# Kernel tuning notes

Hardware: AMD Instinct MI355X
Metric: run time of the kernel (lower is better)

## Reference

```python
import jax, jax.numpy as jnp
import numpy as np

N, E, F, H = 50000, 400000, 128, 512


def setup_inputs() -> dict:
    key = jax.random.key(0)
    k1, k2, k3 = jax.random.split(key, 3)
    x = jax.random.normal(k1, (N, F), dtype=jnp.float32)
    edge_index = jax.random.randint(k2, (2, E), 0, N, dtype=jnp.int64)
    W = jax.random.normal(k3, (H, F), dtype=jnp.float32) * 0.05  # GCNConv linear weight [out, in]
    b = jnp.zeros((H,), dtype=jnp.float32)
    alpha = jnp.full((H,), 0.25, dtype=jnp.float32)  # PReLU default init per channel
    return {"x": x, "edge_index": edge_index, "W": W, "b": b, "alpha": alpha}


def reference(x, edge_index, W, b, alpha):
    n = x.shape[0]
    # GCNConv: linear transform first (no bias inside the matmul)
    h = x @ W.T  # [N, H]
    # add self-loops (GCNConv default add_self_loops=True)
    loops = jnp.arange(n, dtype=edge_index.dtype)
    row = jnp.concatenate([edge_index[0], loops])  # source
    col = jnp.concatenate([edge_index[1], loops])  # target
    # symmetric degree normalization: deg from edge weights (all ones) summed at targets
    deg = jax.ops.segment_sum(jnp.ones_like(col, dtype=h.dtype), col, num_segments=n)
    dinv = jnp.where(deg > 0, jax.lax.rsqrt(jnp.maximum(deg, 1.0)) * (deg > 0), 0.0)
    dinv = jnp.where(deg > 0, 1.0 / jnp.sqrt(jnp.maximum(deg, 1e-12)), 0.0)
    norm = dinv[row] * dinv[col]  # [E+N]
    # gather source features, scale, scatter-add to targets
    msgs = h[row] * norm[:, None]  # [E+N, H] -- the memory-bound gather
    out = jax.ops.segment_sum(msgs, col, num_segments=n) + b  # [N, H]
    # PReLU with per-channel alpha
    return jnp.where(out > 0, out, alpha * out)
```

## Files before the change

kernel.cpp:

```cpp
#include <hip/hip_runtime.h>


#define F_IN 128
#define H_OUT 512

typedef __bf16 bf16x8 __attribute__((ext_vector_type(8)));
typedef float  f32x4  __attribute__((ext_vector_type(4)));

__global__ __launch_bounds__(256) void prep_kernel(const float* __restrict__ W,
                                                   __bf16* __restrict__ Wb, int nw8,
                                                   const float* __restrict__ x,
                                                   __bf16* __restrict__ xs, int nx8,
                                                   const int* __restrict__ col,
                                                   unsigned* __restrict__ deg,
                                                   unsigned* __restrict__ pos, int E,
                                                   int NWB, int NXB) {
    const int b = blockIdx.x, t = threadIdx.x;
    if (b < NWB) {
        int i = b * 256 + t;
        if (i >= nw8) return;
        float4 a0 = ((const float4*)W)[i * 2];
        float4 a1 = ((const float4*)W)[i * 2 + 1];
        bf16x8 v;
        v[0] = (__bf16)a0.x; v[1] = (__bf16)a0.y; v[2] = (__bf16)a0.z; v[3] = (__bf16)a0.w;
        v[4] = (__bf16)a1.x; v[5] = (__bf16)a1.y; v[6] = (__bf16)a1.z; v[7] = (__bf16)a1.w;
        ((bf16x8*)Wb)[i] = v;
    } else if (b < NWB + NXB) {
        int i = (b - NWB) * 256 + t;
        if (i >= nx8) return;
        float4 a0 = ((const float4*)x)[i * 2];
        float4 a1 = ((const float4*)x)[i * 2 + 1];
        bf16x8 v;
        v[0] = (__bf16)a0.x; v[1] = (__bf16)a0.y; v[2] = (__bf16)a0.z; v[3] = (__bf16)a0.w;
        v[4] = (__bf16)a1.x; v[5] = (__bf16)a1.y; v[6] = (__bf16)a1.z; v[7] = (__bf16)a1.w;
        ((bf16x8*)xs)[i] = v;
    } else {
        int e = (b - NWB - NXB) * 256 + t;
        if (e < E) pos[e] = atomicAdd(&deg[col[e]], 1u);
    }
}

__global__ __launch_bounds__(256) void assign_kernel(const unsigned* __restrict__ deg,
                                                     unsigned* __restrict__ total,
                                                     int* __restrict__ rowptr,
                                                     float* __restrict__ dinv, int n) {
    const int i = blockIdx.x * 256 + threadIdx.x;
    const int lane = threadIdx.x & 63;
    unsigned d = (i < n) ? deg[i] : 0u;
    unsigned da = (d + 7u) & ~7u;
    unsigned x = da;
    #pragma unroll
    for (int o = 1; o < 64; o <<= 1) {
        unsigned y = __shfl_up(x, (unsigned)o, 64);
        if (lane >= o) x += y;
    }
    unsigned tot = __shfl(x, 63, 64);
    unsigned wb = 0;
    if (lane == 63) wb = atomicAdd(total, tot);
    wb = __shfl(wb, 63, 64);
    if (i < n) {
        rowptr[i] = (int)(wb + x - da);
        dinv[i]   = rsqrtf((float)(d + 1u));
    }
}

__global__ __launch_bounds__(256) void fill_csr_kernel(const int* __restrict__ row,
                                                       const int* __restrict__ col,
                                                       const unsigned* __restrict__ pos,
                                                       const int* __restrict__ rowptr,
                                                       int* __restrict__ adj, int E) {
    int e = blockIdx.x * 256 + threadIdx.x;
    if (e >= E) return;
    adj[rowptr[col[e]] + (int)pos[e]] = row[e];
}

__global__ __launch_bounds__(256) void gather_agg_kernel(const int* __restrict__ rowptr,
                                                         const unsigned* __restrict__ deg,
                                                         const int* __restrict__ adj,
                                                         const __bf16* __restrict__ xs,
                                                         const float* __restrict__ dinv,
                                                         __bf16* __restrict__ ag, int N) {
    const int t = threadIdx.x;
    const int node = blockIdx.x * 16 + (t >> 4);
    if (node >= N) return;
    const int li = t & 15;

    const bf16x8* xs8 = (const bf16x8*)xs;
    const float dvn = dinv[node];
    bf16x8 sv = xs8[(size_t)node * 16 + li];
    float acc[8];
    #pragma unroll
    for (int q = 0; q < 8; ++q) acc[q] = dvn * (float)sv[q];

    const int s = rowptr[node];
    const int e = s + (int)deg[node];
    for (int j = s; j < e; j += 8) {
        int4 ra = *(const int4*)(adj + j);
        int4 rb = *(const int4*)(adj + j + 4);
        int rr[8];
        rr[0] = ra.x; rr[1] = ra.y; rr[2] = ra.z; rr[3] = ra.w;
        rr[4] = rb.x; rr[5] = rb.y; rr[6] = rb.z; rr[7] = rb.w;
        float wgt[8]; bf16x8 v[8];
        #pragma unroll
        for (int u = 0; u < 8; ++u) {
            const bool ok = (j + u) < e;
            const int r = ok ? rr[u] : node;
            wgt[u] = ok ? dinv[r] : 0.0f;
            v[u]   = xs8[(size_t)r * 16 + li];
        }
        #pragma unroll
        for (int u = 0; u < 8; ++u) {
            #pragma unroll
            for (int q = 0; q < 8; ++q) acc[q] += wgt[u] * (float)v[u][q];
        }
    }

    bf16x8 o;
    #pragma unroll
    for (int q = 0; q < 8; ++q) o[q] = (__bf16)(acc[q] * dvn);
    ((bf16x8*)ag)[(size_t)node * 16 + li] = o;
}

__global__ __launch_bounds__(256) void gemm_mfma_kernel(const __bf16* __restrict__ ag,
                                                        const __bf16* __restrict__ Wb,
                                                        const float* __restrict__ bias,
                                                        const float* __restrict__ alpha,
                                                        float* __restrict__ out, int N) {
    __shared__ __bf16 As[128][136];
    __shared__ __bf16 Bs[128][136];

    const int rb = blockIdx.x * 128;
    const int cb = blockIdx.y * 128;
    const int t  = threadIdx.x;

    #pragma unroll
    for (int i = 0; i < 8; ++i) {
        int c  = i * 256 + t;
        int r  = c >> 4;
        int k8 = (c & 15) * 8;
        bf16x8 v;
        #pragma unroll
        for (int j = 0; j < 8; ++j) v[j] = (__bf16)0.0f;
        if (rb + r < N) v = *(const bf16x8*)(ag + (size_t)(rb + r) * F_IN + k8);
        *(bf16x8*)&As[r][k8] = v;
    }
    #pragma unroll
    for (int i = 0; i < 8; ++i) {
        int c  = i * 256 + t;
        int r  = c >> 4;
        int k8 = (c & 15) * 8;
        bf16x8 v = *(const bf16x8*)(Wb + (size_t)(cb + r) * F_IN + k8);
        *(bf16x8*)&Bs[r][k8] = v;
    }
    __syncthreads();

    const int w    = t >> 6;
    const int lane = t & 63;
    const int lrow = lane & 15;
    const int lk   = (lane >> 4) * 8;

    f32x4 acc[2][8] = {};
    #pragma unroll
    for (int ks = 0; ks < 4; ++ks) {
        const int k0 = ks * 32 + lk;
        bf16x8 a0 = *(const bf16x8*)&As[w * 32 + lrow][k0];
        bf16x8 a1 = *(const bf16x8*)&As[w * 32 + 16 + lrow][k0];
        #pragma unroll
        for (int tn = 0; tn < 8; ++tn) {
            bf16x8 bfr = *(const bf16x8*)&Bs[tn * 16 + lrow][k0];
            acc[0][tn] = __builtin_amdgcn_mfma_f32_16x16x32_bf16(a0, bfr, acc[0][tn], 0, 0, 0);
            acc[1][tn] = __builtin_amdgcn_mfma_f32_16x16x32_bf16(a1, bfr, acc[1][tn], 0, 0, 0);
        }
    }

    float bb[8], aa[8];
    #pragma unroll
    for (int tn = 0; tn < 8; ++tn) {
        int n = cb + tn * 16 + lrow;
        bb[tn] = bias[n];
        aa[tn] = alpha[n];
    }
    const int rloc = (lane >> 4) * 4;
    #pragma unroll
    for (int tm = 0; tm < 2; ++tm) {
        #pragma unroll
        for (int r = 0; r < 4; ++r) {
            int m = rb + w * 32 + tm * 16 + rloc + r;
            if (m >= N) continue;
            #pragma unroll
            for (int tn = 0; tn < 8; ++tn) {
                int n = cb + tn * 16 + lrow;
                float v = acc[tm][tn][r] + bb[tn];
                v = v > 0.f ? v : aa[tn] * v;
                out[(size_t)m * H_OUT + n] = v;
            }
        }
    }
}

extern "C" void kernel_launch(void* const* d_in, const int* in_sizes, int n_in,
                              void* d_out, int out_size, void* d_ws, size_t ws_size,
                              hipStream_t stream) {
    const float* x     = (const float*)d_in[0];
    const int*   ei    = (const int*)d_in[1];
    const float* W     = (const float*)d_in[2];
    const float* b     = (const float*)d_in[3];
    const float* alpha = (const float*)d_in[4];
    float*       out   = (float*)d_out;

    const int N = in_sizes[0] / F_IN;
    const int E = in_sizes[1] / 2;
    const int* row = ei;
    const int* col = ei + E;

    char* wsb = (char*)d_ws;
    size_t off = 0;
    __bf16* xs = (__bf16*)(wsb + off);  off += (size_t)N * F_IN * 2;     off = (off + 63) & ~(size_t)63;
    __bf16* ag = (__bf16*)(wsb + off);  off += (size_t)N * F_IN * 2;     off = (off + 63) & ~(size_t)63;
    __bf16* Wb = (__bf16*)(wsb + off);  off += (size_t)H_OUT * F_IN * 2; off = (off + 63) & ~(size_t)63;
    unsigned* deg    = (unsigned*)(wsb + off);  off += (size_t)(N + 1) * 4;
    float*    dinv   = (float*)(wsb + off);     off += (size_t)N * 4;
    int*      rowptr = (int*)(wsb + off);       off += (size_t)N * 4;
    off = (off + 63) & ~(size_t)63;
    unsigned* pos = (unsigned*)(wsb + off);     off += (size_t)E * 4;
    off = (off + 63) & ~(size_t)63;
    int* adj = (int*)(wsb + off);
    unsigned* total = deg + N;

    const int nw8 = H_OUT * F_IN / 8;
    const int nx8 = N * F_IN / 8;
    const int NWB = (nw8 + 255) / 256;
    const int NXB = (nx8 + 255) / 256;
    const int NEB = (E + 255) / 256;

    hipMemsetAsync(deg, 0, (size_t)(N + 1) * 4, stream);
    prep_kernel<<<NWB + NXB + NEB, 256, 0, stream>>>(W, Wb, nw8, x, xs, nx8,
                                                     col, deg, pos, E, NWB, NXB);
    assign_kernel<<<(N + 255) / 256, 256, 0, stream>>>(deg, total, rowptr, dinv, N);
    fill_csr_kernel<<<(E + 255) / 256, 256, 0, stream>>>(row, col, pos, rowptr, adj, E);
    gather_agg_kernel<<<(N + 15) / 16, 256, 0, stream>>>(rowptr, deg, adj, xs, dinv, ag, N);
    dim3 ggrid((N + 127) / 128, H_OUT / 128);
    gemm_mfma_kernel<<<ggrid, 256, 0, stream>>>(ag, Wb, b, alpha, out, N);
}
```

Measured before the change: 210.7 us.

## Fuse neighbor aggregation into the MFMA GEMM, keeping aggregated rows in LDS

The separate gather-aggregate kernel and GEMM kernel are merged. Each 128-row block aggregates its nodes' neighbor features straight into shared memory, then loops over all four 128-column weight tiles, producing every output column for those rows. This removes the bf16 intermediate write and read to global memory plus one launch, and each aggregated tile is read once instead of four times. In exchange the grid shrinks to about 391 blocks doing serialized gather work, which lowers parallelism and latency hiding for the irregular gather, and W tiles are reloaded per block.

```diff
diff --git a/kernel.cpp b/kernel.cpp
--- a/kernel.cpp
+++ b/kernel.cpp
@@ -74,83 +74,61 @@
     adj[rowptr[col[e]] + (int)pos[e]] = row[e];
 }
 
-__global__ __launch_bounds__(256) void gather_agg_kernel(const int* __restrict__ rowptr,
-                                                         const unsigned* __restrict__ deg,
-                                                         const int* __restrict__ adj,
-                                                         const __bf16* __restrict__ xs,
-                                                         const float* __restrict__ dinv,
-                                                         __bf16* __restrict__ ag, int N) {
-    const int t = threadIdx.x;
-    const int node = blockIdx.x * 16 + (t >> 4);
-    if (node >= N) return;
-    const int li = t & 15;
-
-    const bf16x8* xs8 = (const bf16x8*)xs;
-    const float dvn = dinv[node];
-    bf16x8 sv = xs8[(size_t)node * 16 + li];
-    float acc[8];
-    #pragma unroll
-    for (int q = 0; q < 8; ++q) acc[q] = dvn * (float)sv[q];
-
-    const int s = rowptr[node];
-    const int e = s + (int)deg[node];
-    for (int j = s; j < e; j += 8) {
-        int4 ra = *(const int4*)(adj + j);
-        int4 rb = *(const int4*)(adj + j + 4);
-        int rr[8];
-        rr[0] = ra.x; rr[1] = ra.y; rr[2] = ra.z; rr[3] = ra.w;
-        rr[4] = rb.x; rr[5] = rb.y; rr[6] = rb.z; rr[7] = rb.w;
-        float wgt[8]; bf16x8 v[8];
-        #pragma unroll
-        for (int u = 0; u < 8; ++u) {
-            const bool ok = (j + u) < e;
-            const int r = ok ? rr[u] : node;
-            wgt[u] = ok ? dinv[r] : 0.0f;
-            v[u]   = xs8[(size_t)r * 16 + li];
-        }
-        #pragma unroll
-        for (int u = 0; u < 8; ++u) {
-            #pragma unroll
-            for (int q = 0; q < 8; ++q) acc[q] += wgt[u] * (float)v[u][q];
-        }
-    }
-
-    bf16x8 o;
-    #pragma unroll
-    for (int q = 0; q < 8; ++q) o[q] = (__bf16)(acc[q] * dvn);
-    ((bf16x8*)ag)[(size_t)node * 16 + li] = o;
-}
-
-__global__ __launch_bounds__(256) void gemm_mfma_kernel(const __bf16* __restrict__ ag,
-                                                        const __bf16* __restrict__ Wb,
-                                                        const float* __restrict__ bias,
-                                                        const float* __restrict__ alpha,
-                                                        float* __restrict__ out, int N) {
+__global__ __launch_bounds__(256) void fused_agg_gemm_kernel(
+        const int* __restrict__ rowptr, const unsigned* __restrict__ deg,
+        const int* __restrict__ adj, const __bf16* __restrict__ xs,
+        const float* __restrict__ dinv, const __bf16* __restrict__ Wb,
+        const float* __restrict__ bias, const float* __restrict__ alpha,
+        float* __restrict__ out, int N) {
     __shared__ __bf16 As[128][136];
     __shared__ __bf16 Bs[128][136];
 
     const int rb = blockIdx.x * 128;
-    const int cb = blockIdx.y * 128;
     const int t  = threadIdx.x;
-
-    #pragma unroll
-    for (int i = 0; i < 8; ++i) {
-        int c  = i * 256 + t;
-        int r  = c >> 4;
-        int k8 = (c & 15) * 8;
-        bf16x8 v;
-        #pragma unroll
-        for (int j = 0; j < 8; ++j) v[j] = (__bf16)0.0f;
-        if (rb + r < N) v = *(const bf16x8*)(ag + (size_t)(rb + r) * F_IN + k8);
-        *(bf16x8*)&As[r][k8] = v;
-    }
-    #pragma unroll
-    for (int i = 0; i < 8; ++i) {
-        int c  = i * 256 + t;
-        int r  = c >> 4;
-        int k8 = (c & 15) * 8;
-        bf16x8 v = *(const bf16x8*)(Wb + (size_t)(cb + r) * F_IN + k8);
-        *(bf16x8*)&Bs[r][k8] = v;
+    const int li   = t & 15;
+    const int slot = t >> 4;
+
+    const bf16x8* xs8 = (const bf16x8*)xs;
+
+    for (int nl = slot; nl < 128; nl += 16) {
+        const int node = rb + nl;
+        bf16x8 o;
+        if (node < N) {
+            const float dvn = dinv[node];
+            bf16x8 sv = xs8[(size_t)node * 16 + li];
+            float acc[8];
+            #pragma unroll
+            for (int q = 0; q < 8; ++q) acc[q] = dvn * (float)sv[q];
+
+            const int s = rowptr[node];
+            const int e = s + (int)deg[node];
+            for (int j = s; j < e; j += 8) {
+                int4 ra = *(const int4*)(adj + j);
+                int4 rb4 = *(const int4*)(adj + j + 4);
+                int rr[8];
+                rr[0] = ra.x;  rr[1] = ra.y;  rr[2] = ra.z;  rr[3] = ra.w;
+                rr[4] = rb4.x; rr[5] = rb4.y; rr[6] = rb4.z; rr[7] = rb4.w;
+                float wgt[8]; bf16x8 v[8];
+                #pragma unroll
+                for (int u = 0; u < 8; ++u) {
+                    const bool ok = (j + u) < e;
+                    const int r = ok ? rr[u] : node;
+                    wgt[u] = ok ? dinv[r] : 0.0f;
+                    v[u]   = xs8[(size_t)r * 16 + li];
+                }
+                #pragma unroll
+                for (int u = 0; u < 8; ++u) {
+                    #pragma unroll
+                    for (int q = 0; q < 8; ++q) acc[q] += wgt[u] * (float)v[u][q];
+                }
+            }
+            #pragma unroll
+            for (int q = 0; q < 8; ++q) o[q] = (__bf16)(acc[q] * dvn);
+        } else {
+            #pragma unroll
+            for (int q = 0; q < 8; ++q) o[q] = (__bf16)0.0f;
+        }
+        *(bf16x8*)&As[nl][li * 8] = o;
     }
     __syncthreads();
 
@@ -158,41 +136,61 @@
     const int lane = t & 63;
     const int lrow = lane & 15;
     const int lk   = (lane >> 4) * 8;
-
-    f32x4 acc[2][8] = {};
+    const int rloc = (lane >> 4) * 4;
+
+    bf16x8 af0[4], af1[4];
     #pragma unroll
     for (int ks = 0; ks < 4; ++ks) {
         const int k0 = ks * 32 + lk;
-        bf16x8 a0 = *(const bf16x8*)&As[w * 32 + lrow][k0];
-        bf16x8 a1 = *(const bf16x8*)&As[w * 32 + 16 + lrow][k0];
+        af0[ks] = *(const bf16x8*)&As[w * 32 + lrow][k0];
+        af1[ks] = *(const bf16x8*)&As[w * 32 + 16 + lrow][k0];
+    }
+
+    for (int ct = 0; ct < 4; ++ct) {
+        const int cb = ct * 128;
+        __syncthreads();
+        #pragma unroll
+        for (int i = 0; i < 8; ++i) {
+            int c  = i * 256 + t;
+            int r  = c >> 4;
+            int k8 = (c & 15) * 8;
+            bf16x8 v = *(const bf16x8*)(Wb + (size_t)(cb + r) * F_IN + k8);
+            *(bf16x8*)&Bs[r][k8] = v;
+        }
+        __syncthreads();
+
+        f32x4 acc[2][8] = {};
+        #pragma unroll
+        for (int ks = 0; ks < 4; ++ks) {
+            const int k0 = ks * 32 + lk;
+            #pragma unroll
+            for (int tn = 0; tn < 8; ++tn) {
+                bf16x8 bfr = *(const bf16x8*)&Bs[tn * 16 + lrow][k0];
+                acc[0][tn] = __builtin_amdgcn_mfma_f32_16x16x32_bf16(af0[ks], bfr, acc[0][tn], 0, 0, 0);
+                acc[1][tn] = __builtin_amdgcn_mfma_f32_16x16x32_bf16(af1[ks], bfr, acc[1][tn], 0, 0, 0);
+            }
+        }
+
+        float bb[8], aa[8];
         #pragma unroll
         for (int tn = 0; tn < 8; ++tn) {
-            bf16x8 bfr = *(const bf16x8*)&Bs[tn * 16 + lrow][k0];
-            acc[0][tn] = __builtin_amdgcn_mfma_f32_16x16x32_bf16(a0, bfr, acc[0][tn], 0, 0, 0);
-            acc[1][tn] = __builtin_amdgcn_mfma_f32_16x16x32_bf16(a1, bfr, acc[1][tn], 0, 0, 0);
-        }
-    }
-
-    float bb[8], aa[8];
-    #pragma unroll
-    for (int tn = 0; tn < 8; ++tn) {
-        int n = cb + tn * 16 + lrow;
-        bb[tn] = bias[n];
-        aa[tn] = alpha[n];
-    }
-    const int rloc = (lane >> 4) * 4;
-    #pragma unroll
-    for (int tm = 0; tm < 2; ++tm) {
-        #pragma unroll
-        for (int r = 0; r < 4; ++r) {
-            int m = rb + w * 32 + tm * 16 + rloc + r;
-            if (m >= N) continue;
-            #pragma unroll
-            for (int tn = 0; tn < 8; ++tn) {
-                int n = cb + tn * 16 + lrow;
-                float v = acc[tm][tn][r] + bb[tn];
-                v = v > 0.f ? v : aa[tn] * v;
-                out[(size_t)m * H_OUT + n] = v;
+            int n = cb + tn * 16 + lrow;
+            bb[tn] = bias[n];
+            aa[tn] = alpha[n];
+        }
+        #pragma unroll
+        for (int tm = 0; tm < 2; ++tm) {
+            #pragma unroll
+            for (int r = 0; r < 4; ++r) {
+                int m = rb + w * 32 + tm * 16 + rloc + r;
+                if (m >= N) continue;
+                #pragma unroll
+                for (int tn = 0; tn < 8; ++tn) {
+                    int n = cb + tn * 16 + lrow;
+                    float v = acc[tm][tn][r] + bb[tn];
+                    v = v > 0.f ? v : aa[tn] * v;
+                    out[(size_t)m * H_OUT + n] = v;
+                }
             }
         }
     }
@@ -216,7 +214,6 @@
     char* wsb = (char*)d_ws;
     size_t off = 0;
     __bf16* xs = (__bf16*)(wsb + off);  off += (size_t)N * F_IN * 2;     off = (off + 63) & ~(size_t)63;
-    __bf16* ag = (__bf16*)(wsb + off);  off += (size_t)N * F_IN * 2;     off = (off + 63) & ~(size_t)63;
     __bf16* Wb = (__bf16*)(wsb + off);  off += (size_t)H_OUT * F_IN * 2; off = (off + 63) & ~(size_t)63;
     unsigned* deg    = (unsigned*)(wsb + off);  off += (size_t)(N + 1) * 4;
     float*    dinv   = (float*)(wsb + off);     off += (size_t)N * 4;
@@ -238,7 +235,6 @@
                                                      col, deg, pos, E, NWB, NXB);
     assign_kernel<<<(N + 255) / 256, 256, 0, stream>>>(deg, total, rowptr, dinv, N);
     fill_csr_kernel<<<(E + 255) / 256, 256, 0, stream>>>(row, col, pos, rowptr, adj, E);
-    gather_agg_kernel<<<(N + 15) / 16, 256, 0, stream>>>(rowptr, deg, adj, xs, dinv, ag, N);
-    dim3 ggrid((N + 127) / 128, H_OUT / 128);
-    gemm_mfma_kernel<<<ggrid, 256, 0, stream>>>(ag, Wb, b, alpha, out, N);
-}
+    fused_agg_gemm_kernel<<<(N + 127) / 128, 256, 0, stream>>>(
+        rowptr, deg, adj, xs, dinv, Wb, b, alpha, out, N);
+}
```

Measured after the change: 213.3 us. Within noise of the previous version (+1.2%).

## Loop over all output column tiles per GEMM block, reusing A fragments

Applied to the files above, without the earlier changes.

The GEMM grid drops its column dimension. Each block now loads its 128-row A tile once, keeps the A fragments in registers, and loops over the four 128-column W tiles, reloading Bs in shared memory between passes. This removes the fourfold re-read of the aggregated activations and uses nontemporal stores for the large fp32 output. In exchange there are 4x fewer blocks (about 391), less parallelism to hide latency, and extra barriers around the serial W reloads.

```diff
diff --git a/kernel.cpp b/kernel.cpp
--- a/kernel.cpp
+++ b/kernel.cpp
@@ -95,11 +95,11 @@
     const int s = rowptr[node];
     const int e = s + (int)deg[node];
     for (int j = s; j < e; j += 8) {
-        int4 ra = *(const int4*)(adj + j);
-        int4 rb = *(const int4*)(adj + j + 4);
+        int4 ra  = *(const int4*)(adj + j);
+        int4 rb4 = *(const int4*)(adj + j + 4);
         int rr[8];
-        rr[0] = ra.x; rr[1] = ra.y; rr[2] = ra.z; rr[3] = ra.w;
-        rr[4] = rb.x; rr[5] = rb.y; rr[6] = rb.z; rr[7] = rb.w;
+        rr[0] = ra.x;  rr[1] = ra.y;  rr[2] = ra.z;  rr[3] = ra.w;
+        rr[4] = rb4.x; rr[5] = rb4.y; rr[6] = rb4.z; rr[7] = rb4.w;
         float wgt[8]; bf16x8 v[8];
         #pragma unroll
         for (int u = 0; u < 8; ++u) {
@@ -130,7 +130,6 @@
     __shared__ __bf16 Bs[128][136];
 
     const int rb = blockIdx.x * 128;
-    const int cb = blockIdx.y * 128;
     const int t  = threadIdx.x;
 
     #pragma unroll
@@ -149,8 +148,7 @@
         int c  = i * 256 + t;
         int r  = c >> 4;
         int k8 = (c & 15) * 8;
-        bf16x8 v = *(const bf16x8*)(Wb + (size_t)(cb + r) * F_IN + k8);
-        *(bf16x8*)&Bs[r][k8] = v;
+        *(bf16x8*)&Bs[r][k8] = *(const bf16x8*)(Wb + (size_t)r * F_IN + k8);
     }
     __syncthreads();
 
@@ -158,42 +156,66 @@
     const int lane = t & 63;
     const int lrow = lane & 15;
     const int lk   = (lane >> 4) * 8;
-
-    f32x4 acc[2][8] = {};
+    const int rloc = (lane >> 4) * 4;
+
+    bf16x8 af0[4], af1[4];
     #pragma unroll
     for (int ks = 0; ks < 4; ++ks) {
         const int k0 = ks * 32 + lk;
-        bf16x8 a0 = *(const bf16x8*)&As[w * 32 + lrow][k0];
-        bf16x8 a1 = *(const bf16x8*)&As[w * 32 + 16 + lrow][k0];
+        af0[ks] = *(const bf16x8*)&As[w * 32 + lrow][k0];
+        af1[ks] = *(const bf16x8*)&As[w * 32 + 16 + lrow][k0];
+    }
+
+    #pragma unroll
+    for (int ct = 0; ct < 4; ++ct) {
+        const int cb = ct * 128;
+
+        f32x4 acc[2][8] = {};
+        #pragma unroll
+        for (int ks = 0; ks < 4; ++ks) {
+            const int k0 = ks * 32 + lk;
+            #pragma unroll
+            for (int tn = 0; tn < 8; ++tn) {
+                bf16x8 bfr = *(const bf16x8*)&Bs[tn * 16 + lrow][k0];
+                acc[0][tn] = __builtin_amdgcn_mfma_f32_16x16x32_bf16(af0[ks], bfr, acc[0][tn], 0, 0, 0);
+                acc[1][tn] = __builtin_amdgcn_mfma_f32_16x16x32_bf16(af1[ks], bfr, acc[1][tn], 0, 0, 0);
+            }
+        }
+
+        float bb[8], aa[8];
         #pragma unroll
         for (int tn = 0; tn < 8; ++tn) {
-            bf16x8 bfr = *(const bf16x8*)&Bs[tn * 16 + lrow][k0];
-            acc[0][tn] = __builtin_amdgcn_mfma_f32_16x16x32_bf16(a0, bfr, acc[0][tn], 0, 0, 0);
-            acc[1][tn] = __builtin_amdgcn_mfma_f32_16x16x32_bf16(a1, bfr, acc[1][tn], 0, 0, 0);
-        }
-    }
-
-    float bb[8], aa[8];
-    #pragma unroll
-    for (int tn = 0; tn < 8; ++tn) {
-        int n = cb + tn * 16 + lrow;
-        bb[tn] = bias[n];
-        aa[tn] = alpha[n];
-    }
-    const int rloc = (lane >> 4) * 4;
-    #pragma unroll
-    for (int tm = 0; tm < 2; ++tm) {
-        #pragma unroll
-        for (int r = 0; r < 4; ++r) {
-            int m = rb + w * 32 + tm * 16 + rloc + r;
-            if (m >= N) continue;
-            #pragma unroll
-            for (int tn = 0; tn < 8; ++tn) {
-                int n = cb + tn * 16 + lrow;
-                float v = acc[tm][tn][r] + bb[tn];
-                v = v > 0.f ? v : aa[tn] * v;
-                out[(size_t)m * H_OUT + n] = v;
+            int n = cb + tn * 16 + lrow;
+            bb[tn] = bias[n];
+            aa[tn] = alpha[n];
+        }
+        #pragma unroll
+        for (int tm = 0; tm < 2; ++tm) {
+            #pragma unroll
+            for (int r = 0; r < 4; ++r) {
+                int m = rb + w * 32 + tm * 16 + rloc + r;
+                if (m >= N) continue;
+                #pragma unroll
+                for (int tn = 0; tn < 8; ++tn) {
+                    int n = cb + tn * 16 + lrow;
+                    float v = acc[tm][tn][r] + bb[tn];
+                    v = v > 0.f ? v : aa[tn] * v;
+                    __builtin_nontemporal_store(v, &out[(size_t)m * H_OUT + n]);
+                }
             }
+        }
+
+        if (ct < 3) {
+            __syncthreads();
+            #pragma unroll
+            for (int i = 0; i < 8; ++i) {
+                int c  = i * 256 + t;
+                int r  = c >> 4;
+                int k8 = (c & 15) * 8;
+                *(bf16x8*)&Bs[r][k8] =
+                    *(const bf16x8*)(Wb + (size_t)(cb + 128 + r) * F_IN + k8);
+            }
+            __syncthreads();
         }
     }
 }
@@ -239,6 +261,5 @@
     assign_kernel<<<(N + 255) / 256, 256, 0, stream>>>(deg, total, rowptr, dinv, N);
     fill_csr_kernel<<<(E + 255) / 256, 256, 0, stream>>>(row, col, pos, rowptr, adj, E);
     gather_agg_kernel<<<(N + 15) / 16, 256, 0, stream>>>(rowptr, deg, adj, xs, dinv, ag, N);
-    dim3 ggrid((N + 127) / 128, H_OUT / 128);
-    gemm_mfma_kernel<<<ggrid, 256, 0, stream>>>(ag, Wb, b, alpha, out, N);
-}
+    gemm_mfma_kernel<<<(N + 127) / 128, 256, 0, stream>>>(ag, Wb, b, alpha, out, N);
+}
```

Measured after the change: 209.5 us. Within noise of the previous version (-0.6%).
